# Performance work log

Measured on AMD Instinct MI355X. Metric: run time of the kernel, lower is better.

The kernel has to match this reference:

```python
import jax, jax.numpy as jnp
import numpy as np

N, E, T, CIN, COUT = 20000, 160000, 8, 64, 128


def setup_inputs() -> dict:
    key = jax.random.key(0)
    ks = jax.random.split(key, 8)
    x = jax.random.normal(ks[0], (T, N, CIN), jnp.float32)
    edge_index = jax.random.randint(ks[1], (2, E), 0, N)
    edge_weight = jax.random.normal(ks[2], (E,), jnp.float32)
    # temporal Conv1d: kernel 3, xavier-ish small init (gain=0.1 in source)
    tconv_w = jax.random.normal(ks[3], (COUT, CIN, 3), jnp.float32) * 0.02
    tconv_b = jnp.zeros((COUT,), jnp.float32)
    ln_g = jnp.ones((COUT,), jnp.float32)
    ln_b = jnp.zeros((COUT,), jnp.float32)
    # residual 1x1 Conv1d (in != out channels)
    res_w = jax.random.normal(ks[4], (COUT, CIN), jnp.float32) * 0.05
    res_b = jnp.zeros((COUT,), jnp.float32)
    # GCNConv linear weight [out, in] and bias
    gcn_w = jax.random.normal(ks[5], (COUT, COUT), jnp.float32) * 0.05
    gcn_b = jnp.zeros((COUT,), jnp.float32)
    return dict(x=x, edge_index=edge_index, edge_weight=edge_weight,
                tconv_w=tconv_w, tconv_b=tconv_b, ln_g=ln_g, ln_b=ln_b,
                res_w=res_w, res_b=res_b, gcn_w=gcn_w, gcn_b=gcn_b)


def reference(x, edge_index, edge_weight, tconv_w, tconv_b, ln_g, ln_b,
              res_w, res_b, gcn_w, gcn_b):
    Tn, Nn, _ = x.shape
    xc = jnp.transpose(x, (1, 2, 0))  # [N, Cin, T]
    # temporal conv over T (kernel 3, pad 1)
    h = jax.lax.conv_general_dilated(
        xc, tconv_w, window_strides=(1,), padding=[(1, 1)],
        dimension_numbers=('NCH', 'OIH', 'NCH')) + tconv_b[None, :, None]
    h = jnp.transpose(h, (0, 2, 1))  # [N, T, Cout]
    # LayerNorm over channel dim
    mu = h.mean(-1, keepdims=True)
    var = ((h - mu) ** 2).mean(-1, keepdims=True)
    h = (h - mu) * jax.lax.rsqrt(var + 1e-5) * ln_g + ln_b
    h = jax.nn.relu(h)
    # 1x1 residual conv: [N,Cin,T] x [Cout,Cin] -> [N,T,Cout]
    res = jnp.einsum('nct,oc->nto', xc, res_w) + res_b
    xcmb = h + res  # [N, T, Cout]
    # --- GCNConv (PyG): softmax edge weights, self-loops, sym-normalize ---
    ew = jax.nn.softmax(edge_weight)  # softmax over all edges (dim=0)
    row, col = edge_index[0], edge_index[1]
    sl = jnp.arange(Nn)
    row_f = jnp.concatenate([row, sl])
    col_f = jnp.concatenate([col, sl])
    w_f = jnp.concatenate([ew, jnp.ones((Nn,), ew.dtype)])  # self-loop weight 1
    deg = jax.ops.segment_sum(w_f, col_f, num_segments=Nn)
    dinv = jnp.where(deg > 0, jax.lax.rsqrt(jnp.maximum(deg, 1e-12)), 0.0)
    norm = dinv[row_f] * w_f * dinv[col_f]  # [E+N]
    xt = jnp.einsum('ntc,oc->nto', xcmb, gcn_w)  # linear transform, all T at once
    msg = norm[:, None, None] * xt[row_f]        # gather sources: [E+N, T, Cout]
    agg = jax.ops.segment_sum(msg, col_f, num_segments=Nn) + gcn_b
    out = jax.nn.relu(agg)  # [N, T, Cout]
    return jnp.transpose(out, (1, 0, 2))  # [T, N, Cout] == stacked per-t list
```

## Files before the change

### kernel.cpp

```cpp
#include <hip/hip_runtime.h>
#include <math.h>

#define N_NODES 20000
#define E_EDGES 160000
#define T_STEPS 8
#define C_IN    64
#define C_OUT   128

typedef __bf16 bf16x8 __attribute__((ext_vector_type(8)));
typedef float  f32x4  __attribute__((ext_vector_type(4)));
#define MFMA16(a, b, c) __builtin_amdgcn_mfma_f32_16x16x32_bf16((a), (b), (c), 0, 0, 0)

__device__ __forceinline__ unsigned short f2u(float f) {
  __bf16 b = (__bf16)f;
  return __builtin_bit_cast(unsigned short, b);
}
__device__ __forceinline__ unsigned int pack2(float lo, float hi) {
  return (unsigned int)f2u(lo) | ((unsigned int)f2u(hi) << 16);
}

__device__ __forceinline__ float wredSum(float v) {
#pragma unroll
  for (int d = 32; d > 0; d >>= 1) v += __shfl_xor(v, d, 64);
  return v;
}
__device__ __forceinline__ float wredMax(float v) {
#pragma unroll
  for (int d = 32; d > 0; d >>= 1) v = fmaxf(v, __shfl_xor(v, d, 64));
  return v;
}
__device__ __forceinline__ int wredSumI(int v) {
#pragma unroll
  for (int d = 32; d > 0; d >>= 1) v += __shfl_xor(v, d, 64);
  return v;
}
__device__ __forceinline__ float bredSum(float v, float* sm4) {
  __syncthreads();
  v = wredSum(v);
  const int lane = threadIdx.x & 63, wid = threadIdx.x >> 6;
  if (lane == 0) sm4[wid] = v;
  __syncthreads();
  return sm4[0] + sm4[1] + sm4[2] + sm4[3];
}
__device__ __forceinline__ float bredMax(float v, float* sm4) {
  __syncthreads();
  v = wredMax(v);
  const int lane = threadIdx.x & 63, wid = threadIdx.x >> 6;
  if (lane == 0) sm4[wid] = v;
  __syncthreads();
  return fmaxf(fmaxf(sm4[0], sm4[1]), fmaxf(sm4[2], sm4[3]));
}
__device__ __forceinline__ int bredSumI(int v, int* sm4) {
  __syncthreads();
  v = wredSumI(v);
  const int lane = threadIdx.x & 63, wid = threadIdx.x >> 6;
  if (lane == 0) sm4[wid] = v;
  __syncthreads();
  return sm4[0] + sm4[1] + sm4[2] + sm4[3];
}

__global__ __launch_bounds__(256) void k_esoft(const float* __restrict__ w,
                                               float* __restrict__ pm, float* __restrict__ ps) {
  __shared__ float sm4[4];
  float m = -3.4e38f, s = 0.f;
  for (int i = blockIdx.x * 256 + threadIdx.x; i < E_EDGES; i += 256 * 256) {
    const float xw = w[i];
    if (xw > m) { s = s * expf(m - xw) + 1.f; m = xw; }
    else        { s += expf(xw - m); }
  }
  const float M = bredMax(m, sm4);
  const float sp = (s > 0.f) ? s * expf(m - M) : 0.f;
  const float S = bredSum(sp, sm4);
  if (threadIdx.x == 0) { pm[blockIdx.x] = M; ps[blockIdx.x] = S; }
}

__global__ __launch_bounds__(256) void k_edge(const float* __restrict__ w, const int* __restrict__ ei,
                                              const float* __restrict__ pm, const float* __restrict__ ps,
                                              float* __restrict__ ewv, float* __restrict__ deg,
                                              int* __restrict__ cnt) {
  __shared__ float sm4[4];
  const float mloc = pm[threadIdx.x];
  const float mx   = bredMax(mloc, sm4);
  const float sp   = ps[threadIdx.x] * expf(mloc - mx);
  const float sum  = bredSum(sp, sm4);
  const int e = blockIdx.x * 256 + threadIdx.x;
  const float v = expf(w[e] - mx) / sum;
  ewv[e] = v;
  const int c = ei[E_EDGES + e];
  atomicAdd(&deg[c], v);
  atomicAdd(&cnt[c], 1);
}

__global__ __launch_bounds__(256) void k_scan2(const int* __restrict__ cnt, const float* __restrict__ deg,
                                               float* __restrict__ dinv, int* __restrict__ off,
                                               int* __restrict__ cursor) {
  __shared__ int smI[4];
  __shared__ int wpart[4];
  const int tid = threadIdx.x, lane = tid & 63, wid = tid >> 6;
  const int i = blockIdx.x * 256 + tid;
  if (i < N_NODES) dinv[i] = rsqrtf(deg[i]);
  int part = 0;
  const int lim = blockIdx.x * 256;
  for (int j = tid; j < lim; j += 256) part += cnt[j];
  const int base = bredSumI(part, smI);
  const int v = (i < N_NODES) ? cnt[i] : 0;
  int s = v;
#pragma unroll
  for (int d = 1; d < 64; d <<= 1) { const int u = __shfl_up(s, d, 64); if (lane >= d) s += u; }
  if (lane == 63) wpart[wid] = s;
  __syncthreads();
  int add = base;
#pragma unroll
  for (int wv = 0; wv < 4; ++wv) if (wv < wid) add += wpart[wv];
  if (i < N_NODES) { const int excl = add + (s - v); off[i] = excl; cursor[i] = excl; }
  if (i == N_NODES - 1) off[N_NODES] = E_EDGES;
}

__global__ __launch_bounds__(256) void k_norm_scatter(const int* __restrict__ ei, const float* __restrict__ ewv,
                                                      const float* __restrict__ dinv, const float* __restrict__ qsc,
                                                      int* __restrict__ cursor, uint2* __restrict__ srcnrm) {
  const int e = blockIdx.x * 256 + threadIdx.x;
  const int r = ei[e], c = ei[E_EDGES + e];
  const float mul = dinv[r] * ewv[e] * dinv[c] * qsc[r];
  const int pos = atomicAdd(&cursor[c], 1);
  srcnrm[pos] = make_uint2((unsigned int)r, __builtin_bit_cast(unsigned int, mul));
}

__global__ __launch_bounds__(256) void k_wprep(const float* __restrict__ tconv_w, const float* __restrict__ res_w,
                                               const float* __restrict__ gcn_w, const float* __restrict__ res_b,
                                               unsigned int* __restrict__ Bf, float* __restrict__ c2,
                                               float* __restrict__ deg, int* __restrict__ cnt) {
  const int gid = blockIdx.x * 256 + threadIdx.x;
  if (gid < N_NODES) { deg[gid] = 1.0f; cnt[gid] = 0; }
  if (gid < 128) {
    float s = 0.f;
    for (int o = 0; o < 128; ++o) s += gcn_w[gid * 128 + o] * res_b[o];
    c2[gid] = s;
  }
  float v0, v1;
  if (gid < 12288) {
    const int reg = gid & 3, l = (gid >> 2) & 63, ct = (gid >> 8) & 7, ks = gid >> 11;
    const int o = ct * 16 + (l & 15);
    const int k0 = ks * 32 + ((l >> 4) & 3) * 8 + reg * 2;
    const int c0 = k0 & 63, tap0 = k0 >> 6;
    const int c1 = (k0 + 1) & 63, tap1 = (k0 + 1) >> 6;
    v0 = tconv_w[o * 192 + c0 * 3 + tap0];
    v1 = tconv_w[o * 192 + c1 * 3 + tap1];
  } else if (gid < 16384) {
    const int g = gid - 12288;
    const int reg = g & 3, l = (g >> 2) & 63, ct = (g >> 8) & 7, ks = g >> 11;
    const int q = ct * 16 + (l & 15);
    const int k0 = ks * 32 + ((l >> 4) & 3) * 8 + reg * 2;
    float a0 = 0.f, a1 = 0.f;
    for (int o = 0; o < 128; ++o) {
      const float gq = gcn_w[q * 128 + o];
      a0 = fmaf(gq, res_w[o * 64 + k0], a0);
      a1 = fmaf(gq, res_w[o * 64 + k0 + 1], a1);
    }
    v0 = a0; v1 = a1;
  } else {
    const int g = gid - 16384;
    const int reg = g & 3, l = (g >> 2) & 63, ct = (g >> 8) & 7, ks = g >> 11;
    const int o = ct * 16 + (l & 15);
    const int k0 = ks * 32 + ((l >> 4) & 3) * 8 + reg * 2;
    v0 = gcn_w[o * 128 + k0];
    v1 = gcn_w[o * 128 + k0 + 1];
  }
  Bf[gid] = pack2(v0, v1);
}

#define XS_NODE 720
#define XS_SLOT 72
#define AS2_STRIDE 136
__global__ __launch_bounds__(256, 2) void k_fuse(const float* __restrict__ x,
                                                 const float* __restrict__ tconv_b,
                                                 const float* __restrict__ ln_g, const float* __restrict__ ln_b,
                                                 const unsigned int* __restrict__ Bf,
                                                 const float* __restrict__ c2,
                                                 unsigned char* __restrict__ xq,
                                                 float* __restrict__ qsc) {
  const int tid = threadIdx.x, lane = tid & 63, w = tid >> 6;
  const int l15 = lane & 15, lg = lane >> 4;
  const int n0 = blockIdx.x * 8;

  __shared__ __align__(16) unsigned short Xs[8 * XS_NODE];
  __shared__ __align__(16) unsigned short As2[64 * AS2_STRIDE];
  __shared__ float psum[4][64], psq[4][64];
  __shared__ float smu[64], srs[64];
  __shared__ unsigned int nmax[8];

  if (tid < 8) nmax[tid] = 0u;

#pragma unroll
  for (int p = 0; p < 4; ++p) {
    const int chunk = p * 256 + tid;
    const int tq = chunk >> 7, nn = (chunk >> 4) & 7, c4 = chunk & 15;
    const float4 v = *(const float4*)(x + ((size_t)tq * N_NODES + n0 + nn) * C_IN + c4 * 4);
    uint2 pk; pk.x = pack2(v.x, v.y); pk.y = pack2(v.z, v.w);
    *(uint2*)&Xs[nn * XS_NODE + (tq + 1) * XS_SLOT + c4 * 4] = pk;
  }
#pragma unroll
  for (int p = 0; p < 2; ++p) {
    const int i = p * 256 + tid;
    if (i < 288) {
      const int nn = i / 36;
      const int r = i - nn * 36;
      const int sl = (r < 18) ? 0 : 9;
      const int of = ((r < 18) ? r : r - 18) * 4;
      *(uint2*)&Xs[nn * XS_NODE + sl * XS_SLOT + of] = make_uint2(0u, 0u);
    }
  }

  const uint4* Bf4 = (const uint4*)Bf;
  uint4 Bc[2][6], Bw2[2][2];
#pragma unroll
  for (int ct = 0; ct < 2; ++ct) {
    const int ctg = w * 2 + ct;
#pragma unroll
    for (int ks = 0; ks < 6; ++ks) Bc[ct][ks] = Bf4[(ks * 8 + ctg) * 64 + lane];
#pragma unroll
    for (int ks = 0; ks < 2; ++ks) Bw2[ct][ks] = Bf4[3072 + (ks * 8 + ctg) * 64 + lane];
  }
  float cb[2], gv[2], bv[2], cc[2];
#pragma unroll
  for (int ct = 0; ct < 2; ++ct) {
    const int col = w * 32 + ct * 16 + l15;
    cb[ct] = tconv_b[col]; gv[ct] = ln_g[col]; bv[ct] = ln_b[col]; cc[ct] = c2[col];
  }
  __syncthreads();

  f32x4 accC[4][2];
#pragma unroll
  for (int rt = 0; rt < 4; ++rt)
#pragma unroll
    for (int ct = 0; ct < 2; ++ct) accC[rt][ct] = (f32x4)0.f;

#pragma unroll
  for (int ks = 0; ks < 6; ++ks) {
    bf16x8 af[4];
    const int slot = (l15 & 7) + (ks >> 1);
    const int koff = slot * XS_SLOT + (ks & 1) * 32 + lg * 8;
#pragma unroll
    for (int rt = 0; rt < 4; ++rt) {
      const int node = rt * 2 + (l15 >> 3);
      af[rt] = *(const bf16x8*)&Xs[node * XS_NODE + koff];
    }
#pragma unroll
    for (int rt = 0; rt < 4; ++rt)
#pragma unroll
      for (int ct = 0; ct < 2; ++ct)
        accC[rt][ct] = MFMA16(af[rt], __builtin_bit_cast(bf16x8, Bc[ct][ks]), accC[rt][ct]);
  }

#pragma unroll
  for (int rt = 0; rt < 4; ++rt) {
    float s[4], s2[4];
#pragma unroll
    for (int j = 0; j < 4; ++j) {
      const float h0 = accC[rt][0][j] + cb[0];
      const float h1 = accC[rt][1][j] + cb[1];
      accC[rt][0][j] = h0; accC[rt][1][j] = h1;
      s[j] = h0 + h1; s2[j] = h0 * h0 + h1 * h1;
    }
#pragma unroll
    for (int d = 1; d < 16; d <<= 1)
#pragma unroll
      for (int j = 0; j < 4; ++j) { s[j] += __shfl_xor(s[j], d, 64); s2[j] += __shfl_xor(s2[j], d, 64); }
    if (l15 == 0)
#pragma unroll
      for (int j = 0; j < 4; ++j) {
        psum[w][rt * 16 + lg * 4 + j] = s[j];
        psq[w][rt * 16 + lg * 4 + j] = s2[j];
      }
  }
  __syncthreads();
  if (tid < 64) {
    const float S  = psum[0][tid] + psum[1][tid] + psum[2][tid] + psum[3][tid];
    const float S2 = psq[0][tid] + psq[1][tid] + psq[2][tid] + psq[3][tid];
    const float mu = S * (1.f / 128.f);
    const float var = S2 * (1.f / 128.f) - mu * mu;
    smu[tid] = mu; srs[tid] = rsqrtf(var + 1e-5f);
  }
  __syncthreads();

#pragma unroll
  for (int rt = 0; rt < 4; ++rt)
#pragma unroll
    for (int j = 0; j < 4; ++j) {
      const int row = rt * 16 + lg * 4 + j;
      const float mu = smu[row], rs = srs[row];
      const int sw = ((row >> 3) & 1) << 4;
#pragma unroll
      for (int ct = 0; ct < 2; ++ct) {
        float xc = (accC[rt][ct][j] - mu) * rs * gv[ct] + bv[ct];
        xc = fmaxf(xc, 0.f);
        const int col = w * 32 + ct * 16 + l15;
        As2[row * AS2_STRIDE + (col ^ sw)] = f2u(xc);
      }
    }
  __syncthreads();

  uint4 Bg[2][4];
#pragma unroll
  for (int ct = 0; ct < 2; ++ct)
#pragma unroll
    for (int ks = 0; ks < 4; ++ks) Bg[ct][ks] = Bf4[4096 + (ks * 8 + (w * 2 + ct)) * 64 + lane];

  f32x4 accG[4][2];
#pragma unroll
  for (int rt = 0; rt < 4; ++rt)
#pragma unroll
    for (int ct = 0; ct < 2; ++ct) accG[rt][ct] = (f32x4)0.f;

#pragma unroll
  for (int ks = 0; ks < 2; ++ks) {
    bf16x8 af[4];
    const int koff = ((l15 & 7) + 1) * XS_SLOT + ks * 32 + lg * 8;
#pragma unroll
    for (int rt = 0; rt < 4; ++rt) {
      const int node = rt * 2 + (l15 >> 3);
      af[rt] = *(const bf16x8*)&Xs[node * XS_NODE + koff];
    }
#pragma unroll
    for (int rt = 0; rt < 4; ++rt)
#pragma unroll
      for (int ct = 0; ct < 2; ++ct)
        accG[rt][ct] = MFMA16(af[rt], __builtin_bit_cast(bf16x8, Bw2[ct][ks]), accG[rt][ct]);
  }

  const int swr = ((l15 >> 3) & 1) << 4;
#pragma unroll
  for (int ks = 0; ks < 4; ++ks) {
    bf16x8 af[4];
    const int koff = (ks * 32 + lg * 8) ^ swr;
#pragma unroll
    for (int rt = 0; rt < 4; ++rt)
      af[rt] = *(const bf16x8*)&As2[(rt * 16 + l15) * AS2_STRIDE + koff];
#pragma unroll
    for (int rt = 0; rt < 4; ++rt)
#pragma unroll
      for (int ct = 0; ct < 2; ++ct)
        accG[rt][ct] = MFMA16(af[rt], __builtin_bit_cast(bf16x8, Bg[ct][ks]), accG[rt][ct]);
  }

#pragma unroll
  for (int rt = 0; rt < 4; ++rt) {
#pragma unroll
    for (int ct = 0; ct < 2; ++ct)
#pragma unroll
      for (int j = 0; j < 4; ++j) accG[rt][ct][j] += cc[ct];
    const int nn = rt * 2 + (lg >> 1);
    float m = 0.f;
#pragma unroll
    for (int ct = 0; ct < 2; ++ct)
#pragma unroll
      for (int j = 0; j < 4; ++j) m = fmaxf(m, fabsf(accG[rt][ct][j]));
    atomicMax(&nmax[nn], __builtin_bit_cast(unsigned int, m));
  }
  __syncthreads();
  if (tid < 8) qsc[n0 + tid] = __builtin_bit_cast(float, nmax[tid]) * (1.f / 127.f);

  const int t0 = (lg & 1) * 4;
#pragma unroll
  for (int rt = 0; rt < 4; ++rt) {
    const int nn = rt * 2 + (lg >> 1);
    const size_t n = (size_t)(n0 + nn);
    const float mx = __builtin_bit_cast(float, nmax[nn]);
    const float inv = (mx > 0.f) ? 127.f / mx : 0.f;
#pragma unroll
    for (int ct = 0; ct < 2; ++ct) {
      const int col = w * 32 + ct * 16 + l15;
      unsigned int pk8 = 0;
#pragma unroll
      for (int j = 0; j < 4; ++j) {
        const int q = (int)rintf(accG[rt][ct][j] * inv) + 128;
        pk8 |= ((unsigned int)q) << (8 * j);
      }
      *(unsigned int*)(xq + (n * C_OUT + col) * T_STEPS + t0) = pk8;
    }
  }
}

__global__ __launch_bounds__(256) void k_agg(const unsigned char* __restrict__ xq,
                                             const float* __restrict__ qsc,
                                             const uint2* __restrict__ srcnrm,
                                             const int* __restrict__ off, const float* __restrict__ dinv,
                                             const float* __restrict__ gcn_b, float* __restrict__ out) {
  const int tid = threadIdx.x, lane = tid & 63, w = tid >> 6;
  const int j = blockIdx.x * 4 + w;
  const int s = off[j], e = off[j + 1];
  const float d2 = dinv[j] * dinv[j];

  float acc[2][8];
#pragma unroll
  for (int h = 0; h < 2; ++h)
#pragma unroll
    for (int t = 0; t < 8; ++t) acc[h][t] = 0.f;

  float summul;
  {
    const float mul = d2 * qsc[j];
    summul = mul;
    const uint2 qa = *(const uint2*)(xq + ((size_t)j * C_OUT + lane) * T_STEPS);
    const uint2 qb = *(const uint2*)(xq + ((size_t)j * C_OUT + 64 + lane) * T_STEPS);
#pragma unroll
    for (int tt = 0; tt < 4; ++tt) {
      acc[0][tt]     = fmaf((float)((qa.x >> (8 * tt)) & 0xffu), mul, acc[0][tt]);
      acc[0][4 + tt] = fmaf((float)((qa.y >> (8 * tt)) & 0xffu), mul, acc[0][4 + tt]);
      acc[1][tt]     = fmaf((float)((qb.x >> (8 * tt)) & 0xffu), mul, acc[1][tt]);
      acc[1][4 + tt] = fmaf((float)((qb.y >> (8 * tt)) & 0xffu), mul, acc[1][4 + tt]);
    }
  }

  for (int k = s; k < e; ++k) {
    const uint2 sn = srcnrm[k];
    const int r = (int)sn.x;
    const float mul = __builtin_bit_cast(float, sn.y);
    summul += mul;
    const uint2 qa = *(const uint2*)(xq + ((size_t)r * C_OUT + lane) * T_STEPS);
    const uint2 qb = *(const uint2*)(xq + ((size_t)r * C_OUT + 64 + lane) * T_STEPS);
#pragma unroll
    for (int tt = 0; tt < 4; ++tt) {
      acc[0][tt]     = fmaf((float)((qa.x >> (8 * tt)) & 0xffu), mul, acc[0][tt]);
      acc[0][4 + tt] = fmaf((float)((qa.y >> (8 * tt)) & 0xffu), mul, acc[0][4 + tt]);
      acc[1][tt]     = fmaf((float)((qb.x >> (8 * tt)) & 0xffu), mul, acc[1][tt]);
      acc[1][4 + tt] = fmaf((float)((qb.y >> (8 * tt)) & 0xffu), mul, acc[1][4 + tt]);
    }
  }

  const float corr = 128.f * summul;
  const float b0 = gcn_b[lane], b1 = gcn_b[64 + lane];
#pragma unroll
  for (int h = 0; h < 2; ++h) {
    const float bo = h ? b1 : b0;
#pragma unroll
    for (int t = 0; t < 8; ++t) {
      const float v = acc[h][t] - corr + bo;
      out[((size_t)t * N_NODES + j) * C_OUT + h * 64 + lane] = fmaxf(v, 0.f);
    }
  }
}

extern "C" void kernel_launch(void* const* d_in, const int* in_sizes, int n_in,
                              void* d_out, int out_size, void* d_ws, size_t ws_size,
                              hipStream_t stream) {
  (void)in_sizes; (void)n_in; (void)out_size; (void)ws_size;
  const float* x       = (const float*)d_in[0];
  const int*   ei      = (const int*)d_in[1];
  const float* ewt     = (const float*)d_in[2];
  const float* tconv_w = (const float*)d_in[3];
  const float* tconv_b = (const float*)d_in[4];
  const float* ln_g    = (const float*)d_in[5];
  const float* ln_b    = (const float*)d_in[6];
  const float* res_w   = (const float*)d_in[7];
  const float* res_b   = (const float*)d_in[8];
  const float* gcn_w   = (const float*)d_in[9];
  const float* gcn_b   = (const float*)d_in[10];
  float* out = (float*)d_out;

  unsigned char* xq = (unsigned char*)d_ws;
  float* qsc  = (float*)(xq + (size_t)N_NODES * C_OUT * T_STEPS);
  float* c2   = qsc + N_NODES;
  unsigned int* Bf = (unsigned int*)(c2 + 128);
  float* ewv   = (float*)(Bf + 24576);
  float* deg   = ewv + E_EDGES;
  float* dinv  = deg + N_NODES;
  float* pm    = dinv + N_NODES;
  float* ps    = pm + 256;
  int*   cnt    = (int*)(ps + 256);
  int*   off    = cnt + N_NODES;
  int*   cursor = off + N_NODES + 1;
  uint2* srcnrm = (uint2*)(((size_t)(cursor + N_NODES) + 15) & ~(size_t)15);

  const int nblk = (N_NODES + 255) / 256;
  const int eblk = E_EDGES / 256;

  k_wprep<<<96, 256, 0, stream>>>(tconv_w, res_w, gcn_w, res_b, Bf, c2, deg, cnt);
  k_esoft<<<256, 256, 0, stream>>>(ewt, pm, ps);
  k_edge<<<eblk, 256, 0, stream>>>(ewt, ei, pm, ps, ewv, deg, cnt);
  k_scan2<<<nblk, 256, 0, stream>>>(cnt, deg, dinv, off, cursor);
  k_fuse<<<2500, 256, 0, stream>>>(x, tconv_b, ln_g, ln_b, Bf, c2, xq, qsc);
  k_norm_scatter<<<eblk, 256, 0, stream>>>(ei, ewv, dinv, qsc, cursor, srcnrm);
  k_agg<<<N_NODES / 4, 256, 0, stream>>>(xq, qsc, srcnrm, off, dinv, gcn_b, out);
}
```

Baseline: 142.5 us.

## Merge weight-prep and softmax kernels, shuffle max reduction, split aggregation channels

Combines the weight-prep kernel and the edge-softmax partial-reduction kernel into one launch, removing one kernel launch and its dependency gap. In the fused node kernel, the per-node abs-max for quantisation now uses a wave-shuffle reduction plus shared-memory combine instead of shared atomicMax on bit-cast floats. The aggregation kernel now gives each wave 64 channels of a node instead of all 128, so there are twice as many blocks, fewer registers per thread and more parallelism over neighbour gathers. The cost is that edge metadata (srcnrm, off) is read twice per node and one extra __syncthreads is added.

```diff
diff --git a/kernel.cpp b/kernel.cpp
--- a/kernel.cpp
+++ b/kernel.cpp
@@ -59,12 +59,55 @@
   return sm4[0] + sm4[1] + sm4[2] + sm4[3];
 }
 
-__global__ __launch_bounds__(256) void k_esoft(const float* __restrict__ w,
-                                               float* __restrict__ pm, float* __restrict__ ps) {
+__global__ __launch_bounds__(256) void k_prep(const float* __restrict__ tconv_w, const float* __restrict__ res_w,
+                                              const float* __restrict__ gcn_w, const float* __restrict__ res_b,
+                                              const float* __restrict__ ewt,
+                                              unsigned int* __restrict__ Bf, float* __restrict__ c2,
+                                              float* __restrict__ deg, int* __restrict__ cnt,
+                                              float* __restrict__ pm, float* __restrict__ ps) {
+  const int gid = blockIdx.x * 256 + threadIdx.x;
+  if (gid < N_NODES) { deg[gid] = 1.0f; cnt[gid] = 0; }
+  if (gid < 128) {
+    float s = 0.f;
+    for (int o = 0; o < 128; ++o) s += gcn_w[gid * 128 + o] * res_b[o];
+    c2[gid] = s;
+  }
+  if (gid < 24576) {
+    float v0, v1;
+    if (gid < 12288) {
+      const int reg = gid & 3, l = (gid >> 2) & 63, ct = (gid >> 8) & 7, ks = gid >> 11;
+      const int o = ct * 16 + (l & 15);
+      const int k0 = ks * 32 + ((l >> 4) & 3) * 8 + reg * 2;
+      const int c0 = k0 & 63, tap0 = k0 >> 6;
+      const int c1 = (k0 + 1) & 63, tap1 = (k0 + 1) >> 6;
+      v0 = tconv_w[o * 192 + c0 * 3 + tap0];
+      v1 = tconv_w[o * 192 + c1 * 3 + tap1];
+    } else if (gid < 16384) {
+      const int g = gid - 12288;
+      const int reg = g & 3, l = (g >> 2) & 63, ct = (g >> 8) & 7, ks = g >> 11;
+      const int q = ct * 16 + (l & 15);
+      const int k0 = ks * 32 + ((l >> 4) & 3) * 8 + reg * 2;
+      float a0 = 0.f, a1 = 0.f;
+      for (int o = 0; o < 128; ++o) {
+        const float gq = gcn_w[q * 128 + o];
+        a0 = fmaf(gq, res_w[o * 64 + k0], a0);
+        a1 = fmaf(gq, res_w[o * 64 + k0 + 1], a1);
+      }
+      v0 = a0; v1 = a1;
+    } else {
+      const int g = gid - 16384;
+      const int reg = g & 3, l = (g >> 2) & 63, ct = (g >> 8) & 7, ks = g >> 11;
+      const int o = ct * 16 + (l & 15);
+      const int k0 = ks * 32 + ((l >> 4) & 3) * 8 + reg * 2;
+      v0 = gcn_w[o * 128 + k0];
+      v1 = gcn_w[o * 128 + k0 + 1];
+    }
+    Bf[gid] = pack2(v0, v1);
+  }
   __shared__ float sm4[4];
   float m = -3.4e38f, s = 0.f;
   for (int i = blockIdx.x * 256 + threadIdx.x; i < E_EDGES; i += 256 * 256) {
-    const float xw = w[i];
+    const float xw = ewt[i];
     if (xw > m) { s = s * expf(m - xw) + 1.f; m = xw; }
     else        { s += expf(xw - m); }
   }
@@ -126,49 +169,6 @@
   srcnrm[pos] = make_uint2((unsigned int)r, __builtin_bit_cast(unsigned int, mul));
 }
 
-__global__ __launch_bounds__(256) void k_wprep(const float* __restrict__ tconv_w, const float* __restrict__ res_w,
-                                               const float* __restrict__ gcn_w, const float* __restrict__ res_b,
-                                               unsigned int* __restrict__ Bf, float* __restrict__ c2,
-                                               float* __restrict__ deg, int* __restrict__ cnt) {
-  const int gid = blockIdx.x * 256 + threadIdx.x;
-  if (gid < N_NODES) { deg[gid] = 1.0f; cnt[gid] = 0; }
-  if (gid < 128) {
-    float s = 0.f;
-    for (int o = 0; o < 128; ++o) s += gcn_w[gid * 128 + o] * res_b[o];
-    c2[gid] = s;
-  }
-  float v0, v1;
-  if (gid < 12288) {
-    const int reg = gid & 3, l = (gid >> 2) & 63, ct = (gid >> 8) & 7, ks = gid >> 11;
-    const int o = ct * 16 + (l & 15);
-    const int k0 = ks * 32 + ((l >> 4) & 3) * 8 + reg * 2;
-    const int c0 = k0 & 63, tap0 = k0 >> 6;
-    const int c1 = (k0 + 1) & 63, tap1 = (k0 + 1) >> 6;
-    v0 = tconv_w[o * 192 + c0 * 3 + tap0];
-    v1 = tconv_w[o * 192 + c1 * 3 + tap1];
-  } else if (gid < 16384) {
-    const int g = gid - 12288;
-    const int reg = g & 3, l = (g >> 2) & 63, ct = (g >> 8) & 7, ks = g >> 11;
-    const int q = ct * 16 + (l & 15);
-    const int k0 = ks * 32 + ((l >> 4) & 3) * 8 + reg * 2;
-    float a0 = 0.f, a1 = 0.f;
-    for (int o = 0; o < 128; ++o) {
-      const float gq = gcn_w[q * 128 + o];
-      a0 = fmaf(gq, res_w[o * 64 + k0], a0);
-      a1 = fmaf(gq, res_w[o * 64 + k0 + 1], a1);
-    }
-    v0 = a0; v1 = a1;
-  } else {
-    const int g = gid - 16384;
-    const int reg = g & 3, l = (g >> 2) & 63, ct = (g >> 8) & 7, ks = g >> 11;
-    const int o = ct * 16 + (l & 15);
-    const int k0 = ks * 32 + ((l >> 4) & 3) * 8 + reg * 2;
-    v0 = gcn_w[o * 128 + k0];
-    v1 = gcn_w[o * 128 + k0 + 1];
-  }
-  Bf[gid] = pack2(v0, v1);
-}
-
 #define XS_NODE 720
 #define XS_SLOT 72
 #define AS2_STRIDE 136
@@ -187,9 +187,8 @@
   __shared__ __align__(16) unsigned short As2[64 * AS2_STRIDE];
   __shared__ float psum[4][64], psq[4][64];
   __shared__ float smu[64], srs[64];
-  __shared__ unsigned int nmax[8];
-
-  if (tid < 8) nmax[tid] = 0u;
+  __shared__ float pmax4[4][8];
+  __shared__ float smax8[8];
 
 #pragma unroll
   for (int p = 0; p < 4; ++p) {
@@ -349,23 +348,29 @@
     for (int ct = 0; ct < 2; ++ct)
 #pragma unroll
       for (int j = 0; j < 4; ++j) accG[rt][ct][j] += cc[ct];
-    const int nn = rt * 2 + (lg >> 1);
     float m = 0.f;
 #pragma unroll
     for (int ct = 0; ct < 2; ++ct)
 #pragma unroll
       for (int j = 0; j < 4; ++j) m = fmaxf(m, fabsf(accG[rt][ct][j]));
-    atomicMax(&nmax[nn], __builtin_bit_cast(unsigned int, m));
-  }
-  __syncthreads();
-  if (tid < 8) qsc[n0 + tid] = __builtin_bit_cast(float, nmax[tid]) * (1.f / 127.f);
+#pragma unroll
+    for (int d = 1; d < 32; d <<= 1) m = fmaxf(m, __shfl_xor(m, d, 64));
+    if ((lane & 31) == 0) pmax4[w][rt * 2 + (lane >> 5)] = m;
+  }
+  __syncthreads();
+  if (tid < 8) {
+    const float mx = fmaxf(fmaxf(pmax4[0][tid], pmax4[1][tid]), fmaxf(pmax4[2][tid], pmax4[3][tid]));
+    smax8[tid] = mx;
+    qsc[n0 + tid] = mx * (1.f / 127.f);
+  }
+  __syncthreads();
 
   const int t0 = (lg & 1) * 4;
 #pragma unroll
   for (int rt = 0; rt < 4; ++rt) {
     const int nn = rt * 2 + (lg >> 1);
     const size_t n = (size_t)(n0 + nn);
-    const float mx = __builtin_bit_cast(float, nmax[nn]);
+    const float mx = smax8[nn];
     const float inv = (mx > 0.f) ? 127.f / mx : 0.f;
 #pragma unroll
     for (int ct = 0; ct < 2; ++ct) {
@@ -387,28 +392,24 @@
                                              const int* __restrict__ off, const float* __restrict__ dinv,
                                              const float* __restrict__ gcn_b, float* __restrict__ out) {
   const int tid = threadIdx.x, lane = tid & 63, w = tid >> 6;
-  const int j = blockIdx.x * 4 + w;
+  const int j = blockIdx.x * 2 + (w >> 1);
+  const int ch = (w & 1) * 64 + lane;
   const int s = off[j], e = off[j + 1];
   const float d2 = dinv[j] * dinv[j];
 
-  float acc[2][8];
-#pragma unroll
-  for (int h = 0; h < 2; ++h)
-#pragma unroll
-    for (int t = 0; t < 8; ++t) acc[h][t] = 0.f;
+  float acc[8];
+#pragma unroll
+  for (int t = 0; t < 8; ++t) acc[t] = 0.f;
 
   float summul;
   {
     const float mul = d2 * qsc[j];
     summul = mul;
-    const uint2 qa = *(const uint2*)(xq + ((size_t)j * C_OUT + lane) * T_STEPS);
-    const uint2 qb = *(const uint2*)(xq + ((size_t)j * C_OUT + 64 + lane) * T_STEPS);
+    const uint2 q = *(const uint2*)(xq + ((size_t)j * C_OUT + ch) * T_STEPS);
 #pragma unroll
     for (int tt = 0; tt < 4; ++tt) {
-      acc[0][tt]     = fmaf((float)((qa.x >> (8 * tt)) & 0xffu), mul, acc[0][tt]);
-      acc[0][4 + tt] = fmaf((float)((qa.y >> (8 * tt)) & 0xffu), mul, acc[0][4 + tt]);
-      acc[1][tt]     = fmaf((float)((qb.x >> (8 * tt)) & 0xffu), mul, acc[1][tt]);
-      acc[1][4 + tt] = fmaf((float)((qb.y >> (8 * tt)) & 0xffu), mul, acc[1][4 + tt]);
+      acc[tt]     = fmaf((float)((q.x >> (8 * tt)) & 0xffu), mul, acc[tt]);
+      acc[4 + tt] = fmaf((float)((q.y >> (8 * tt)) & 0xffu), mul, acc[4 + tt]);
     }
   }
 
@@ -417,27 +418,20 @@
     const int r = (int)sn.x;
     const float mul = __builtin_bit_cast(float, sn.y);
     summul += mul;
-    const uint2 qa = *(const uint2*)(xq + ((size_t)r * C_OUT + lane) * T_STEPS);
-    const uint2 qb = *(const uint2*)(xq + ((size_t)r * C_OUT + 64 + lane) * T_STEPS);
+    const uint2 q = *(const uint2*)(xq + ((size_t)r * C_OUT + ch) * T_STEPS);
 #pragma unroll
     for (int tt = 0; tt < 4; ++tt) {
-      acc[0][tt]     = fmaf((float)((qa.x >> (8 * tt)) & 0xffu), mul, acc[0][tt]);
-      acc[0][4 + tt] = fmaf((float)((qa.y >> (8 * tt)) & 0xffu), mul, acc[0][4 + tt]);
-      acc[1][tt]     = fmaf((float)((qb.x >> (8 * tt)) & 0xffu), mul, acc[1][tt]);
-      acc[1][4 + tt] = fmaf((float)((qb.y >> (8 * tt)) & 0xffu), mul, acc[1][4 + tt]);
+      acc[tt]     = fmaf((float)((q.x >> (8 * tt)) & 0xffu), mul, acc[tt]);
+      acc[4 + tt] = fmaf((float)((q.y >> (8 * tt)) & 0xffu), mul, acc[4 + tt]);
     }
   }
 
   const float corr = 128.f * summul;
-  const float b0 = gcn_b[lane], b1 = gcn_b[64 + lane];
-#pragma unroll
-  for (int h = 0; h < 2; ++h) {
-    const float bo = h ? b1 : b0;
-#pragma unroll
-    for (int t = 0; t < 8; ++t) {
-      const float v = acc[h][t] - corr + bo;
-      out[((size_t)t * N_NODES + j) * C_OUT + h * 64 + lane] = fmaxf(v, 0.f);
-    }
+  const float b = gcn_b[ch];
+#pragma unroll
+  for (int t = 0; t < 8; ++t) {
+    const float v = acc[t] - corr + b;
+    out[((size_t)t * N_NODES + j) * C_OUT + ch] = fmaxf(v, 0.f);
   }
 }
 
@@ -475,11 +469,10 @@
   const int nblk = (N_NODES + 255) / 256;
   const int eblk = E_EDGES / 256;
 
-  k_wprep<<<96, 256, 0, stream>>>(tconv_w, res_w, gcn_w, res_b, Bf, c2, deg, cnt);
-  k_esoft<<<256, 256, 0, stream>>>(ewt, pm, ps);
+  k_prep<<<256, 256, 0, stream>>>(tconv_w, res_w, gcn_w, res_b, ewt, Bf, c2, deg, cnt, pm, ps);
   k_edge<<<eblk, 256, 0, stream>>>(ewt, ei, pm, ps, ewv, deg, cnt);
   k_scan2<<<nblk, 256, 0, stream>>>(cnt, deg, dinv, off, cursor);
   k_fuse<<<2500, 256, 0, stream>>>(x, tconv_b, ln_g, ln_b, Bf, c2, xq, qsc);
   k_norm_scatter<<<eblk, 256, 0, stream>>>(ei, ewv, dinv, qsc, cursor, srcnrm);
-  k_agg<<<N_NODES / 4, 256, 0, stream>>>(xq, qsc, srcnrm, off, dinv, gcn_b, out);
-}
+  k_agg<<<N_NODES / 2, 256, 0, stream>>>(xq, qsc, srcnrm, off, dinv, gcn_b, out);
+}
```

Result: no change. 145.1 us (+1.8%).
